# Performance work log

Hardware: AMD Instinct MI355X
Metric: run time of the kernel (lower is better)

The kernel has to match this reference:

```python
import jax, jax.numpy as jnp
import numpy as np

NUM_HEAD = 16
D = 1024
HEAD_DIM = D // NUM_HEAD
EPS = 1e-5


def setup_inputs() -> dict:
    key = jax.random.key(0)
    ks = jax.random.split(key, 7)
    B, S = 2, 2048
    s = 1.0 / np.sqrt(D)
    return {
        "x": jax.random.normal(ks[0], (B, S, D), dtype=jnp.float32),
        "wq": jax.random.uniform(ks[1], (D, D), jnp.float32, -s, s),
        "bq": jax.random.uniform(ks[2], (D,), jnp.float32, -s, s),
        "wk": jax.random.uniform(ks[3], (D, D), jnp.float32, -s, s),
        "bk": jax.random.uniform(ks[4], (D,), jnp.float32, -s, s),
        "wv": jax.random.uniform(ks[5], (D, D), jnp.float32, -s, s),
        "bv": jax.random.uniform(ks[6], (D,), jnp.float32, -s, s),
        "gamma": jnp.ones((D,), jnp.float32),
        "beta": jnp.zeros((D,), jnp.float32),
    }


def reference(x, wq, bq, wk, bk, wv, bv, gamma, beta):
    B, S, Dm = x.shape
    # Linear: x @ W^T + b (torch convention), then split heads -> [B, H, S, hd]
    def proj(w, b):
        y = jnp.einsum("bsd,ed->bse", x, w) + b
        return y.reshape(B, S, NUM_HEAD, HEAD_DIM).transpose(0, 2, 1, 3)

    q = proj(wq, bq)
    k = proj(wk, bk)
    v = proj(wv, bv)

    scores = jnp.einsum("bhqd,bhkd->bhqk", q, k) / np.sqrt(HEAD_DIM).astype(x.dtype)
    attn = jax.nn.softmax(scores, axis=-1)
    out = jnp.einsum("bhqk,bhkd->bhqd", attn, v)
    out = out.transpose(0, 2, 1, 3).reshape(B, S, Dm)

    out = out + x
    mu = jnp.mean(out, axis=-1, keepdims=True)
    var = jnp.var(out, axis=-1, keepdims=True)
    out = (out - mu) * jax.lax.rsqrt(var + EPS) * gamma + beta
    return out
```

## Files before the change

### kernel.cpp

```cpp
#include <hip/hip_runtime.h>

typedef unsigned short u16;
typedef unsigned int   u32;
typedef __bf16 bf16x8 __attribute__((ext_vector_type(8)));
typedef float  f32x4  __attribute__((ext_vector_type(4)));

#define D_MODEL 1024
#define SEQ     2048
#define NHEAD   16
#define HD      64
#define SOFTMAX_SCL 0.18033688011112042f

__device__ __forceinline__ u16 f2bf(float f) {
    u32 u;
    __builtin_memcpy(&u, &f, 4);
    u32 r = (u + 0x7fffu + ((u >> 16) & 1u)) >> 16;
    return (u16)r;
}

__device__ __forceinline__ void async_copy16(const u16* g, u16* l) {
    __builtin_amdgcn_global_load_lds(
        (__attribute__((address_space(1))) void*)g,
        (__attribute__((address_space(3))) void*)l, 16, 0, 0);
}

__global__ __launch_bounds__(256) void f32_to_bf16(
    const float* __restrict__ src, u16* __restrict__ dst, int n4)
{
    int i = blockIdx.x * 256 + threadIdx.x;
    if (i >= n4) return;
    float4 a = ((const float4*)src)[i];
    ushort4 o;
    o.x = f2bf(a.x); o.y = f2bf(a.y); o.z = f2bf(a.z); o.w = f2bf(a.w);
    ((ushort4*)dst)[i] = o;
}

__global__ __launch_bounds__(256) void qkv_gemm(
    const u16* __restrict__ xb,
    const u16* __restrict__ wqb, const float* __restrict__ bq,
    const u16* __restrict__ wkb, const float* __restrict__ bk,
    const u16* __restrict__ wvb, const float* __restrict__ bv,
    u16* __restrict__ qb, u16* __restrict__ kb, u16* __restrict__ vt)
{
    const int z = blockIdx.z;
    const u16* Ap; const u16* Bp;
    int m0, n0;
    if (z < 2) {
        Ap = xb; Bp = (z == 1) ? wkb : wqb;
        m0 = blockIdx.y * 128;
        n0 = blockIdx.x * 128;
    } else {
        Ap = wvb; Bp = xb;
        m0 = blockIdx.x * 128;
        n0 = blockIdx.y * 128;
    }

    __shared__ u16 As[128 * 64];
    __shared__ u16 Bs[128 * 64];

    const int tid  = threadIdx.x;
    const int wave = tid >> 6;
    const int lane = tid & 63;
    const int quad = lane >> 4;
    const int l16  = lane & 15;
    const int wm   = wave >> 1;
    const int wn   = wave & 1;
    const int swz  = l16 & 7;

    int rr[4], co[4];
#pragma unroll
    for (int t = 0; t < 4; ++t) {
        int ch = (wave * 4 + t) * 64 + lane;
        rr[t] = ch >> 3;
        co[t] = ((ch & 7) ^ (rr[t] & 7)) * 8;
    }

    f32x4 acc[4][4] = {};

    for (int kt = 0; kt < D_MODEL; kt += 64) {
        __syncthreads();
#pragma unroll
        for (int t = 0; t < 4; ++t) {
            int chbase = (wave * 4 + t) * 64;
            async_copy16(Ap + (size_t)(m0 + rr[t]) * D_MODEL + kt + co[t], As + chbase * 8);
            async_copy16(Bp + (size_t)(n0 + rr[t]) * D_MODEL + kt + co[t], Bs + chbase * 8);
        }
        __syncthreads();

#pragma unroll
        for (int kc = 0; kc < 2; ++kc) {
            bf16x8 af[4], bf_[4];
#pragma unroll
            for (int i = 0; i < 4; ++i)
                af[i] = *(const bf16x8*)&As[(wm * 64 + i * 16 + l16) * 64 + (((kc * 4 + quad) ^ swz) << 3)];
#pragma unroll
            for (int j = 0; j < 4; ++j)
                bf_[j] = *(const bf16x8*)&Bs[(wn * 64 + j * 16 + l16) * 64 + (((kc * 4 + quad) ^ swz) << 3)];
#pragma unroll
            for (int i = 0; i < 4; ++i)
#pragma unroll
                for (int j = 0; j < 4; ++j)
                    acc[i][j] = __builtin_amdgcn_mfma_f32_16x16x32_bf16(af[i], bf_[j], acc[i][j], 0, 0, 0);
        }
    }

    if (z < 2) {
        u16* out = (z == 1) ? kb : qb;
        const float* bi = (z == 1) ? bk : bq;
        const float scl = (z == 1) ? 1.0f : SOFTMAX_SCL;
#pragma unroll
        for (int j = 0; j < 4; ++j) {
            int col = n0 + wn * 64 + j * 16 + l16;
            float bias = bi[col];
            int colbase = col & ~63;
            int dc  = (col >> 3) & 7;
            int dlo = col & 7;
#pragma unroll
            for (int i = 0; i < 4; ++i) {
#pragma unroll
                for (int r = 0; r < 4; ++r) {
                    int row = m0 + wm * 64 + i * 16 + quad * 4 + r;
                    size_t addr = (size_t)row * D_MODEL + colbase + ((dc ^ (row & 7)) << 3) + dlo;
                    out[addr] = f2bf((acc[i][j][r] + bias) * scl);
                }
            }
        }
    } else {
#pragma unroll
        for (int i = 0; i < 4; ++i) {
#pragma unroll
            for (int r = 0; r < 4; ++r) {
                int feat = m0 + wm * 64 + i * 16 + quad * 4 + r;
                float bias = bv[feat];
                int h = feat >> 6, d = feat & 63;
#pragma unroll
                for (int j = 0; j < 4; ++j) {
                    int tok = n0 + wn * 64 + j * 16 + l16;
                    int b = tok >> 11, s = tok & 2047;
                    size_t addr = ((size_t)(b * NHEAD + h) * HD + d) * SEQ
                                + (s & ~63) + (((((s >> 3) & 7) ^ (d & 7)) << 3)) + (s & 7);
                    vt[addr] = f2bf(acc[i][j][r] + bias);
                }
            }
        }
    }
}

__global__ __launch_bounds__(256) void attn_kernel(
    const u16* __restrict__ qb, const u16* __restrict__ kb, const u16* __restrict__ vtg,
    float* __restrict__ ob)
{
    const int b  = blockIdx.z;
    const int h  = blockIdx.y;
    const int q0 = blockIdx.x * 128;

    const int tid  = threadIdx.x;
    const int wave = tid >> 6;
    const int lane = tid & 63;
    const int quad = lane >> 4;
    const int l16  = lane & 15;
    const int swz  = l16 & 7;

    __shared__ u16 Ks[64 * 64];
    __shared__ u16 Vt[64 * 64];
    __shared__ u16 Ps[8 * 1024];

    const size_t kbase = (size_t)b * SEQ * D_MODEL + h * 64;
    const size_t vbase = (size_t)(b * NHEAD + h) * HD * SEQ;

    bf16x8 aq[2][2];
#pragma unroll
    for (int rb = 0; rb < 2; ++rb) {
        const int qrow = q0 + wave * 32 + rb * 16 + l16;
        const u16* qrp = qb + (size_t)qrow * D_MODEL + h * 64;
        aq[rb][0] = *(const bf16x8*)(qrp + ((quad ^ swz) << 3));
        aq[rb][1] = *(const bf16x8*)(qrp + (((4 + quad) ^ swz) << 3));
    }

    const int r0 = tid >> 3, r1 = (tid + 256) >> 3;
    const int cs8 = (tid & 7) * 8;
    const u16* kg0 = kb + kbase + (size_t)r0 * D_MODEL + cs8;
    const u16* kg1 = kb + kbase + (size_t)r1 * D_MODEL + cs8;
    const u16* vg0 = vtg + vbase + (size_t)r0 * SEQ + cs8;
    const u16* vg1 = vtg + vbase + (size_t)r1 * SEQ + cs8;
    u16* KsD0 = Ks + wave * 512;
    u16* KsD1 = Ks + 2048 + wave * 512;
    u16* VtD0 = Vt + wave * 512;
    u16* VtD1 = Vt + 2048 + wave * 512;

    f32x4 oacc[2][4] = {};
    float lsum[2][4] = {};

    for (int kt = 0; kt < SEQ; kt += 64) {
        __syncthreads();
        async_copy16(kg0, KsD0);
        async_copy16(kg1, KsD1);
        async_copy16(vg0, VtD0);
        async_copy16(vg1, VtD1);
        kg0 += 64 * D_MODEL; kg1 += 64 * D_MODEL;
        vg0 += 64;           vg1 += 64;
        __syncthreads();

        f32x4 sacc[2][4] = {};
#pragma unroll
        for (int c = 0; c < 2; ++c) {
            bf16x8 bk_[4];
#pragma unroll
            for (int nb = 0; nb < 4; ++nb)
                bk_[nb] = *(const bf16x8*)&Ks[(nb * 16 + l16) * 64 + (((c * 4 + quad) ^ swz) << 3)];
#pragma unroll
            for (int rb = 0; rb < 2; ++rb)
#pragma unroll
                for (int nb = 0; nb < 4; ++nb)
                    sacc[rb][nb] = __builtin_amdgcn_mfma_f32_16x16x32_bf16(aq[rb][c], bk_[nb], sacc[rb][nb], 0, 0, 0);
        }

#pragma unroll
        for (int rb = 0; rb < 2; ++rb)
#pragma unroll
            for (int r = 0; r < 4; ++r)
#pragma unroll
                for (int nb = 0; nb < 4; ++nb) {
                    float e = exp2f(sacc[rb][nb][r]);
                    lsum[rb][r] += e;
                    u32 bits;
                    __builtin_memcpy(&bits, &e, 4);
                    Ps[wave * 2048 + rb * 1024 + r * 256 + nb * 64 + lane] = (u16)(bits >> 16);
                }

#pragma unroll
        for (int c = 0; c < 2; ++c) {
            bf16x8 ap[2];
#pragma unroll
            for (int rb = 0; rb < 2; ++rb)
                ap[rb] = *(const bf16x8*)&Ps[wave * 2048 + rb * 1024 + (l16 & 3) * 256
                                             + (c * 2 + (quad >> 1)) * 64
                                             + (l16 >> 2) * 16 + (quad & 1) * 8];
            bf16x8 bv_[4];
#pragma unroll
            for (int nb = 0; nb < 4; ++nb)
                bv_[nb] = *(const bf16x8*)&Vt[(nb * 16 + l16) * 64 + (((c * 4 + quad) ^ swz) << 3)];
#pragma unroll
            for (int rb = 0; rb < 2; ++rb)
#pragma unroll
                for (int nb = 0; nb < 4; ++nb)
                    oacc[rb][nb] = __builtin_amdgcn_mfma_f32_16x16x32_bf16(ap[rb], bv_[nb], oacc[rb][nb], 0, 0, 0);
        }
    }

#pragma unroll
    for (int rb = 0; rb < 2; ++rb)
#pragma unroll
        for (int r = 0; r < 4; ++r) {
            float s = lsum[rb][r];
            s += __shfl_xor(s, 1, 64);
            s += __shfl_xor(s, 2, 64);
            s += __shfl_xor(s, 4, 64);
            s += __shfl_xor(s, 8, 64);
            float inv = 1.0f / s;
            int row = q0 + wave * 32 + rb * 16 + quad * 4 + r;
#pragma unroll
            for (int nb = 0; nb < 4; ++nb) {
                int d = nb * 16 + l16;
                ob[((size_t)b * SEQ + row) * D_MODEL + h * 64 + d] = oacc[rb][nb][r] * inv;
            }
        }
}

__global__ __launch_bounds__(256) void add_ln(
    const float* __restrict__ attn, const float* __restrict__ x,
    const float* __restrict__ gamma, const float* __restrict__ beta,
    float* __restrict__ out)
{
    const int row = blockIdx.x;
    const int tid = threadIdx.x;
    const size_t rb = (size_t)row * D_MODEL;

    float4 a  = ((const float4*)(attn + rb))[tid];
    float4 xb = ((const float4*)(x + rb))[tid];

    float v[4];
    v[0] = a.x + xb.x;
    v[1] = a.y + xb.y;
    v[2] = a.z + xb.z;
    v[3] = a.w + xb.w;

    float s  = v[0] + v[1] + v[2] + v[3];
    float s2 = v[0]*v[0] + v[1]*v[1] + v[2]*v[2] + v[3]*v[3];
#pragma unroll
    for (int off = 1; off < 64; off <<= 1) {
        s  += __shfl_xor(s, off, 64);
        s2 += __shfl_xor(s2, off, 64);
    }

    __shared__ float red[2][4];
    int wave = tid >> 6, lane = tid & 63;
    if (lane == 0) { red[0][wave] = s; red[1][wave] = s2; }
    __syncthreads();
    float st  = red[0][0] + red[0][1] + red[0][2] + red[0][3];
    float s2t = red[1][0] + red[1][1] + red[1][2] + red[1][3];

    float mu   = st * (1.0f / D_MODEL);
    float var  = s2t * (1.0f / D_MODEL) - mu * mu;
    float rstd = rsqrtf(var + 1e-5f);

    float4 g  = ((const float4*)(gamma))[tid];
    float4 bt = ((const float4*)(beta))[tid];
    float4 o;
    o.x = (v[0] - mu) * rstd * g.x + bt.x;
    o.y = (v[1] - mu) * rstd * g.y + bt.y;
    o.z = (v[2] - mu) * rstd * g.z + bt.z;
    o.w = (v[3] - mu) * rstd * g.w + bt.w;
    ((float4*)(out + rb))[tid] = o;
}

extern "C" void kernel_launch(void* const* d_in, const int* in_sizes, int n_in,
                              void* d_out, int out_size, void* d_ws, size_t ws_size,
                              hipStream_t stream) {
    const float* x     = (const float*)d_in[0];
    const float* wq    = (const float*)d_in[1];
    const float* bq    = (const float*)d_in[2];
    const float* wk    = (const float*)d_in[3];
    const float* bk    = (const float*)d_in[4];
    const float* wv    = (const float*)d_in[5];
    const float* bv    = (const float*)d_in[6];
    const float* gamma = (const float*)d_in[7];
    const float* beta  = (const float*)d_in[8];
    float* outp = (float*)d_out;

    char* ws = (char*)d_ws;
    u16*   xb  = (u16*)(ws);
    u16*   wqb = (u16*)(ws + ((size_t)8  << 20));
    u16*   wkb = (u16*)(ws + ((size_t)10 << 20));
    u16*   wvb = (u16*)(ws + ((size_t)12 << 20));
    u16*   qb  = (u16*)(ws + ((size_t)16 << 20));
    u16*   kb  = (u16*)(ws + ((size_t)24 << 20));
    u16*   vt  = (u16*)(ws + ((size_t)32 << 20));
    float* ab  = (float*)(ws + ((size_t)40 << 20));

    const int NX = (2 * SEQ * D_MODEL) / 4;
    const int NW = (D_MODEL * D_MODEL) / 4;
    f32_to_bf16<<<dim3((NX + 255) / 256), 256, 0, stream>>>(x,  xb,  NX);
    f32_to_bf16<<<dim3((NW + 255) / 256), 256, 0, stream>>>(wq, wqb, NW);
    f32_to_bf16<<<dim3((NW + 255) / 256), 256, 0, stream>>>(wk, wkb, NW);
    f32_to_bf16<<<dim3((NW + 255) / 256), 256, 0, stream>>>(wv, wvb, NW);

    qkv_gemm<<<dim3(8, 32, 3), 256, 0, stream>>>(xb, wqb, bq, wkb, bk, wvb, bv, qb, kb, vt);
    attn_kernel<<<dim3(SEQ / 128, NHEAD, 2), 256, 0, stream>>>(qb, kb, vt, ab);
    add_ln<<<dim3(2 * SEQ), 256, 0, stream>>>(ab, x, gamma, beta, outp);
}
```

Baseline: 214.8 us.

## Double-buffer K/V tiles in attention, remap grid, fuse bf16 conversions

The attention kernel now double-buffers its K and V LDS tiles. It issues the async global-to-LDS copy for the next tile before computing on the current one, which removes one barrier per iteration. The grid becomes 1D with batch and head in the low bits, so each XCD in the round-robin dispatch handles a fixed set of heads, which may improve L2 reuse of K/V. The four f32-to-bf16 conversion launches are merged into one kernel that branches on index range. The cost is double the K/V LDS footprint, which could lower occupancy, plus reliance on the barrier's implicit wait for the async copies.

```diff
diff --git a/kernel.cpp b/kernel.cpp
--- a/kernel.cpp
+++ b/kernel.cpp
@@ -24,15 +24,24 @@
         (__attribute__((address_space(3))) void*)l, 16, 0, 0);
 }
 
-__global__ __launch_bounds__(256) void f32_to_bf16(
-    const float* __restrict__ src, u16* __restrict__ dst, int n4)
+#define NX4 ((2 * SEQ * D_MODEL) / 4)
+#define NW4 ((D_MODEL * D_MODEL) / 4)
+__global__ __launch_bounds__(256) void conv_all(
+    const float* __restrict__ x,  const float* __restrict__ wq,
+    const float* __restrict__ wk, const float* __restrict__ wv,
+    u16* __restrict__ xb, u16* __restrict__ wqb,
+    u16* __restrict__ wkb, u16* __restrict__ wvb)
 {
     int i = blockIdx.x * 256 + threadIdx.x;
-    if (i >= n4) return;
-    float4 a = ((const float4*)src)[i];
+    const float* src; u16* dst; int off;
+    if (i < NX4)            { src = x;  dst = xb;  off = i; }
+    else if (i < NX4 + NW4) { src = wq; dst = wqb; off = i - NX4; }
+    else if (i < NX4 + 2 * NW4) { src = wk; dst = wkb; off = i - NX4 - NW4; }
+    else                    { src = wv; dst = wvb; off = i - NX4 - 2 * NW4; }
+    float4 a = ((const float4*)src)[off];
     ushort4 o;
     o.x = f2bf(a.x); o.y = f2bf(a.y); o.z = f2bf(a.z); o.w = f2bf(a.w);
-    ((ushort4*)dst)[i] = o;
+    ((ushort4*)dst)[off] = o;
 }
 
 __global__ __launch_bounds__(256) void qkv_gemm(
@@ -150,9 +159,11 @@
     const u16* __restrict__ qb, const u16* __restrict__ kb, const u16* __restrict__ vtg,
     float* __restrict__ ob)
 {
-    const int b  = blockIdx.z;
-    const int h  = blockIdx.y;
-    const int q0 = blockIdx.x * 128;
+    const int bid = blockIdx.x;
+    const int bh  = bid & 31;
+    const int b   = bh >> 4;
+    const int h   = bh & 15;
+    const int q0  = (bid >> 5) * 128;
 
     const int tid  = threadIdx.x;
     const int wave = tid >> 6;
@@ -161,8 +172,8 @@
     const int l16  = lane & 15;
     const int swz  = l16 & 7;
 
-    __shared__ u16 Ks[64 * 64];
-    __shared__ u16 Vt[64 * 64];
+    __shared__ u16 KsB[2][4096];
+    __shared__ u16 VtB[2][4096];
     __shared__ u16 Ps[8 * 1024];
 
     const size_t kbase = (size_t)b * SEQ * D_MODEL + h * 64;
@@ -183,23 +194,31 @@
     const u16* kg1 = kb + kbase + (size_t)r1 * D_MODEL + cs8;
     const u16* vg0 = vtg + vbase + (size_t)r0 * SEQ + cs8;
     const u16* vg1 = vtg + vbase + (size_t)r1 * SEQ + cs8;
-    u16* KsD0 = Ks + wave * 512;
-    u16* KsD1 = Ks + 2048 + wave * 512;
-    u16* VtD0 = Vt + wave * 512;
-    u16* VtD1 = Vt + 2048 + wave * 512;
+    const int wofs = wave * 512;
 
     f32x4 oacc[2][4] = {};
     float lsum[2][4] = {};
 
-    for (int kt = 0; kt < SEQ; kt += 64) {
+    async_copy16(kg0, &KsB[0][wofs]);
+    async_copy16(kg1, &KsB[0][2048 + wofs]);
+    async_copy16(vg0, &VtB[0][wofs]);
+    async_copy16(vg1, &VtB[0][2048 + wofs]);
+    kg0 += 64 * D_MODEL; kg1 += 64 * D_MODEL;
+    vg0 += 64;           vg1 += 64;
+
+    for (int t = 0; t < SEQ / 64; ++t) {
         __syncthreads();
-        async_copy16(kg0, KsD0);
-        async_copy16(kg1, KsD1);
-        async_copy16(vg0, VtD0);
-        async_copy16(vg1, VtD1);
-        kg0 += 64 * D_MODEL; kg1 += 64 * D_MODEL;
-        vg0 += 64;           vg1 += 64;
-        __syncthreads();
+        if (t < SEQ / 64 - 1) {
+            const int nb_ = (t + 1) & 1;
+            async_copy16(kg0, &KsB[nb_][wofs]);
+            async_copy16(kg1, &KsB[nb_][2048 + wofs]);
+            async_copy16(vg0, &VtB[nb_][wofs]);
+            async_copy16(vg1, &VtB[nb_][2048 + wofs]);
+            kg0 += 64 * D_MODEL; kg1 += 64 * D_MODEL;
+            vg0 += 64;           vg1 += 64;
+        }
+        const u16* Ks = KsB[t & 1];
+        const u16* Vt = VtB[t & 1];
 
         f32x4 sacc[2][4] = {};
 #pragma unroll
@@ -338,14 +357,9 @@
     u16*   vt  = (u16*)(ws + ((size_t)32 << 20));
     float* ab  = (float*)(ws + ((size_t)40 << 20));
 
-    const int NX = (2 * SEQ * D_MODEL) / 4;
-    const int NW = (D_MODEL * D_MODEL) / 4;
-    f32_to_bf16<<<dim3((NX + 255) / 256), 256, 0, stream>>>(x,  xb,  NX);
-    f32_to_bf16<<<dim3((NW + 255) / 256), 256, 0, stream>>>(wq, wqb, NW);
-    f32_to_bf16<<<dim3((NW + 255) / 256), 256, 0, stream>>>(wk, wkb, NW);
-    f32_to_bf16<<<dim3((NW + 255) / 256), 256, 0, stream>>>(wv, wvb, NW);
-
+    conv_all<<<dim3((NX4 + 3 * NW4) / 256), 256, 0, stream>>>(
+        x, wq, wk, wv, xb, wqb, wkb, wvb);
     qkv_gemm<<<dim3(8, 32, 3), 256, 0, stream>>>(xb, wqb, bq, wkb, bk, wvb, bv, qb, kb, vt);
-    attn_kernel<<<dim3(SEQ / 128, NHEAD, 2), 256, 0, stream>>>(qb, kb, vt, ab);
+    attn_kernel<<<dim3(512), 256, 0, stream>>>(qb, kb, vt, ab);
     add_ln<<<dim3(2 * SEQ), 256, 0, stream>>>(ab, x, gamma, beta, outp);
 }
```

Measured after the change: 208.9 us. 2.7% less time.
